# Kernel optimization log

Hardware: AMD Instinct MI355X
Metric: run time of the kernel (lower is better)

The kernel has to match this reference:

```python
import jax, jax.numpy as jnp
import numpy as np

NUM_HEADS = 16
HEAD_DIM = 64
EMBED_DIM = 1024
MASKED_BIAS = -10000.0


def setup_inputs() -> dict:
    key = jax.random.key(0)
    ks = jax.random.split(key, 4)
    B, S, D = 4, 1024, EMBED_DIM
    scale = 0.02
    return {
        "hidden_states": jax.random.normal(ks[0], (B, S, D), dtype=jnp.float32),
        "c_attn_w": jax.random.normal(ks[1], (D, 3 * D), dtype=jnp.float32) * scale,
        "c_attn_b": jnp.zeros((3 * D,), dtype=jnp.float32),
        "c_proj_w": jax.random.normal(ks[2], (D, D), dtype=jnp.float32) * scale,
        "c_proj_b": jnp.zeros((D,), dtype=jnp.float32),
        "affine_w": jnp.ones((D,), dtype=jnp.float32),
        "affine_b": jnp.zeros((D,), dtype=jnp.float32),
    }


def reference(hidden_states, c_attn_w, c_attn_b, c_proj_w, c_proj_b, affine_w, affine_b):
    B, S, D = hidden_states.shape
    H, Dh = NUM_HEADS, HEAD_DIM
    # c_attn (GPT2 Conv1D): x @ W + b -> [B,S,3D], split into q,k,v
    qkv = hidden_states @ c_attn_w + c_attn_b
    q, k, v = jnp.split(qkv, 3, axis=-1)
    # split heads -> [B,H,S,Dh]
    def split_heads(t):
        return t.reshape(B, S, H, Dh).transpose(0, 2, 1, 3)
    q, k, v = split_heads(q), split_heads(k), split_heads(v)
    # QK^T scaled by 1/sqrt(head_dim) (value.size(-1)**0.5)
    attn_weights = jnp.einsum("bhqd,bhkd->bhqk", q, k) / jnp.asarray(
        Dh, hidden_states.dtype) ** 0.5
    # causal mask via where with -10000 sentinel (eager GPT2 semantics)
    causal = jnp.tril(jnp.ones((S, S), dtype=bool))[None, None]
    attn_weights = jnp.where(causal, attn_weights,
                             jnp.asarray(MASKED_BIAS, attn_weights.dtype))
    attn_weights = jax.nn.softmax(attn_weights, axis=-1)
    # attn dropout = identity in eval
    attn_output = jnp.einsum("bhqk,bhkd->bhqd", attn_weights, v)
    # merge heads -> [B,S,D]
    attn_output = attn_output.transpose(0, 2, 1, 3).reshape(B, S, D)
    # c_proj (Conv1D), resid dropout identity, then affine
    attn_output = attn_output @ c_proj_w + c_proj_b
    attn_output = attn_output * affine_w + affine_b
    return attn_output
```

## Files before the change

kernel.cpp:

```cpp
#include <hip/hip_runtime.h>


typedef __attribute__((ext_vector_type(4))) float  fx4;
typedef __attribute__((ext_vector_type(4))) short  sx4;
typedef __attribute__((ext_vector_type(8))) short  sx8;
typedef __attribute__((ext_vector_type(4))) float  f32x4;
typedef __attribute__((ext_vector_type(8))) __bf16 bf16x8;

#define DEVI static __device__ __forceinline__
#define BARRIER asm volatile("s_barrier" ::: "memory")
#define VMCNT0  asm volatile("s_waitcnt vmcnt(0)" ::: "memory")

DEVI short f2bf(float f) {
  unsigned u = __builtin_bit_cast(unsigned, f);
  u = (u + 0x7FFFu + ((u >> 16) & 1u)) >> 16;
  return (short)u;
}

DEVI fx4 mfma16(sx8 a, sx8 b, fx4 c) {
  return __builtin_amdgcn_mfma_f32_16x16x32_bf16(
      __builtin_bit_cast(bf16x8, a), __builtin_bit_cast(bf16x8, b), c, 0, 0, 0);
}

DEVI void gl_lds16(const void* g, void* l) {
  __builtin_amdgcn_global_load_lds(
      (const __attribute__((address_space(1))) void*)g,
      (__attribute__((address_space(3))) void*)l, 16, 0, 0);
}

__global__ __launch_bounds__(256) void prologue(
    const float* __restrict__ hs, short* __restrict__ hsb,
    const float* __restrict__ caw, short* __restrict__ wqkvt,
    const float* __restrict__ cpw, short* __restrict__ wprojt) {
  __shared__ float tbuf[32][33];
  const int bid = blockIdx.x, tid = threadIdx.x;
  if (bid < 4096) {
    const float* in;
    short* out;
    int C, bx, by;
    if (bid < 3072) {
      in = caw; out = wqkvt; C = 3072; bx = bid % 96; by = bid / 96;
    } else {
      int t = bid - 3072;
      in = cpw; out = wprojt; C = 1024; bx = t & 31; by = t >> 5;
    }
    const int R = 1024;
    int tx = tid & 31, ty = tid >> 5;
    int r0 = by * 32, c0 = bx * 32;
#pragma unroll
    for (int i = 0; i < 4; ++i)
      tbuf[ty + i * 8][tx] = in[(size_t)(r0 + ty + i * 8) * C + c0 + tx];
    __syncthreads();
#pragma unroll
    for (int i = 0; i < 4; ++i)
      out[(size_t)(c0 + ty + i * 8) * R + r0 + tx] = f2bf(tbuf[tx][ty + i * 8]);
  } else {
    int i = (bid - 4096) * 256 + tid;
    f32x4 v = *(const f32x4*)&hs[(size_t)i * 4];
    sx4 o;
#pragma unroll
    for (int j = 0; j < 4; ++j) o[j] = f2bf(v[j]);
    *(sx4*)&hsb[(size_t)i * 4] = o;
  }
}

__global__ __launch_bounds__(512, 4) void gemm_qkv(
    const short* __restrict__ A, const short* __restrict__ Bt,
    const float* __restrict__ bias, short* __restrict__ Qg,
    short* __restrict__ Kg, short* __restrict__ Vtg) {
  __shared__ __align__(16) short As[2][64][64];
  __shared__ __align__(16) short Bs[2][128][64];
  const int tid = threadIdx.x, lane = tid & 63, w = tid >> 6;
  const int bid = blockIdx.x;
  const int x = bid & 7, loc = bid >> 3;
  const int bn = (x & 3) * 3 + loc % 3;
  const int bm = (x >> 2) * 16 + loc / 3;
  const int wm = w >> 2, wn = w & 3;
  const int c0 = lane & 15, g = lane >> 4;
  const int l3 = lane >> 3, l7 = lane & 7;
  const int slog = l7 ^ l3;
  const int par = slog >> 2, gg = slog & 3;
  const int K = 1024;
  fx4 acc[4][4] = {};

  auto STAGE = [&](int bf, int kt) {
    {
      int row = w * 16 + l3 * 2 + par;
      gl_lds16(&A[(size_t)(bm * 128 + row) * K + kt + gg * 8], &As[bf][w * 8][0]);
    }
#pragma unroll
    for (int i = 0; i < 2; ++i) {
      int ch = w * 2 + i;
      int row = ch * 16 + l3 * 2 + par;
      gl_lds16(&Bt[(size_t)(bn * 256 + row) * K + kt + gg * 8], &Bs[bf][ch * 8][0]);
    }
  };

  STAGE(0, 0);
  VMCNT0;
  BARRIER;
  for (int t = 0; t < 32; ++t) {
    const int bf = t & 1;
    if (t + 1 < 32) STAGE(bf ^ 1, (t + 1) * 32);

    sx8 af[4], bfr[4];
#pragma unroll
    for (int m = 0; m < 4; ++m) {
      int r = wm * 64 + m * 16 + c0, pr = r >> 1;
      int sl = (((r & 1) << 2) | g) ^ (pr & 7);
      af[m] = *(const sx8*)&As[bf][pr][sl * 8];
    }
#pragma unroll
    for (int n = 0; n < 4; ++n) {
      int r = wn * 64 + n * 16 + c0, pr = r >> 1;
      int sl = (((r & 1) << 2) | g) ^ (pr & 7);
      bfr[n] = *(const sx8*)&Bs[bf][pr][sl * 8];
    }
    __builtin_amdgcn_s_setprio(1);
#pragma unroll
    for (int m = 0; m < 4; ++m)
#pragma unroll
      for (int n = 0; n < 4; ++n) acc[m][n] = mfma16(af[m], bfr[n], acc[m][n]);
    __builtin_amdgcn_s_setprio(0);

    if (t + 1 < 32) {
      VMCNT0;
      BARRIER;
    }
  }

  const float SCALE_Q = 0.125f * 1.4426950408889634f;
#pragma unroll
  for (int m = 0; m < 4; ++m) {
#pragma unroll
    for (int n = 0; n < 4; ++n) {
      int col = bn * 256 + wn * 64 + n * 16 + c0;
      int row0 = bm * 128 + wm * 64 + m * 16 + g * 4;
      float bv = bias[col];
      int b = row0 >> 10, s0 = row0 & 1023;
      if (col < 1024) {
        int h = col >> 6, d = col & 63;
        size_t base = ((size_t)(b * 16 + h) * 1024) * 64 + d;
#pragma unroll
        for (int r = 0; r < 4; ++r)
          Qg[base + (size_t)(s0 + r) * 64] = f2bf((acc[m][n][r] + bv) * SCALE_Q);
      } else if (col < 2048) {
        int c = col - 1024, h = c >> 6, d = c & 63;
        size_t base = ((size_t)(b * 16 + h) * 1024) * 64 + d;
#pragma unroll
        for (int r = 0; r < 4; ++r)
          Kg[base + (size_t)(s0 + r) * 64] = f2bf(acc[m][n][r] + bv);
      } else {
        int c = col - 2048, h = c >> 6, d = c & 63;
        sx4 v;
#pragma unroll
        for (int r = 0; r < 4; ++r) v[r] = f2bf(acc[m][n][r] + bv);
        *(sx4*)&Vtg[((size_t)(b * 16 + h) * 64 + d) * 1024 + s0] = v;
      }
    }
  }
}

__global__ __launch_bounds__(512, 4) void gemm_proj(
    const short* __restrict__ A, const short* __restrict__ Bt,
    const float* __restrict__ bias, const float* __restrict__ aw,
    const float* __restrict__ ab, float* __restrict__ Out) {
  __shared__ __align__(16) short As[2][128][64];
  __shared__ __align__(16) short Bs[2][128][64];
  const int tid = threadIdx.x, lane = tid & 63, w = tid >> 6;
  const int bid = blockIdx.x;
  const int x = bid & 7, k = bid >> 3;
  const int bn = x, bm = k;
  const int wm = w >> 2, wn = w & 3;
  const int c0 = lane & 15, g = lane >> 4;
  const int lr8 = lane >> 3, ls8 = (lane & 7) ^ lr8;
  const int K = 1024, N = 1024;
  fx4 acc[4][2] = {};

  auto STAGE = [&](int bf, int kt) {
#pragma unroll
    for (int i = 0; i < 2; ++i) {
      int idx = w * 2 + i;
      gl_lds16(&A[(size_t)(bm * 128 + idx * 8 + lr8) * K + kt + ls8 * 8],
               &As[bf][idx * 8][0]);
      gl_lds16(&Bt[(size_t)(bn * 128 + idx * 8 + lr8) * K + kt + ls8 * 8],
               &Bs[bf][idx * 8][0]);
    }
  };

  STAGE(0, 0);
  VMCNT0;
  BARRIER;
  for (int t = 0; t < 16; ++t) {
    const int bf = t & 1;
    if (t + 1 < 16) STAGE(bf ^ 1, (t + 1) * 64);
#pragma unroll
    for (int kk = 0; kk < 2; ++kk) {
      sx8 af[4], bfr[2];
      int sb = kk * 4 + g;
#pragma unroll
      for (int m = 0; m < 4; ++m) {
        int row = wm * 64 + m * 16 + c0;
        af[m] = *(const sx8*)&As[bf][row][(sb ^ (row & 7)) * 8];
      }
#pragma unroll
      for (int n = 0; n < 2; ++n) {
        int row = wn * 32 + n * 16 + c0;
        bfr[n] = *(const sx8*)&Bs[bf][row][(sb ^ (row & 7)) * 8];
      }
#pragma unroll
      for (int m = 0; m < 4; ++m)
#pragma unroll
        for (int n = 0; n < 2; ++n) acc[m][n] = mfma16(af[m], bfr[n], acc[m][n]);
    }
    if (t + 1 < 16) {
      VMCNT0;
      BARRIER;
    }
  }

#pragma unroll
  for (int m = 0; m < 4; ++m) {
#pragma unroll
    for (int n = 0; n < 2; ++n) {
      int col = bn * 128 + wn * 32 + n * 16 + c0;
      int row0 = bm * 128 + wm * 64 + m * 16 + g * 4;
      float bv = bias[col], wv = aw[col], av = ab[col];
#pragma unroll
      for (int r = 0; r < 4; ++r)
        Out[(size_t)(row0 + r) * N + col] = (acc[m][n][r] + bv) * wv + av;
    }
  }
}

__global__ __launch_bounds__(256, 4) void attn_kernel(const short* __restrict__ Qg,
                                                      const short* __restrict__ Kg,
                                                      const short* __restrict__ Vtg,
                                                      short* __restrict__ AO) {
  __shared__ __align__(16) short Ks[2][64][64];
  __shared__ __align__(16) short Vts[2][64][64];
  __shared__ __align__(16) short Ps[4][16 * 64];
  const int tid = threadIdx.x, lane = tid & 63, w = tid >> 6;
  const int bid = blockIdx.x;
  const int u = bid >> 8, v = bid & 255, bh = v >> 2, jj = v & 3;
  const int qt = (u == 0) ? jj : (u == 1) ? 7 - jj : (u == 2) ? 8 + jj : 15 - jj;
  const int b = bh >> 4, h = bh & 15;
  const int c0 = lane & 15, g = lane >> 4;
  const int lr8 = lane >> 3, ls8 = (lane & 7) ^ lr8;
  const int q0 = qt * 64 + w * 16;
  const short* Qp = Qg + (size_t)bh * 65536;
  const short* Kp = Kg + (size_t)bh * 65536;
  const short* Vp = Vtg + (size_t)bh * 65536;
  short* pbase = &Ps[w][0];
  const int s8 = (c0 & 7) * 8;

  sx8 qf[2];
#pragma unroll
  for (int kk = 0; kk < 2; ++kk)
    qf[kk] = *(const sx8*)&Qp[(size_t)(q0 + c0) * 64 + kk * 32 + g * 8];

  fx4 o[4] = {};
  float mrun = -1e30f, lrun = 0.f;
  const int q_glob = q0 + c0;

  auto STAGE = [&](int bf, int kv0) {
#pragma unroll
    for (int i = 0; i < 2; ++i) {
      int idx = w * 2 + i;
      gl_lds16(&Kp[(size_t)(kv0 + idx * 8 + lr8) * 64 + ls8 * 8], &Ks[bf][idx * 8][0]);
    }
#pragma unroll
    for (int i = 0; i < 2; ++i) {
      int idx = w * 2 + i;
      gl_lds16(&Vp[(size_t)(idx * 8 + lr8) * 1024 + kv0 + ls8 * 8], &Vts[bf][idx * 8][0]);
    }
  };

  STAGE(0, 0);
  VMCNT0;
  BARRIER;
  for (int t = 0; t <= qt; ++t) {
    const int kv0 = t * 64;
    const int bf = t & 1;
    const bool more = t < qt;
    if (more) STAGE(bf ^ 1, kv0 + 64);

    fx4 st[4];
    __builtin_amdgcn_s_setprio(1);
#pragma unroll
    for (int mf = 0; mf < 4; ++mf) {
      int row = mf * 16 + c0;
      sx8 kf0 = *(const sx8*)&Ks[bf][row][(g ^ (row & 7)) * 8];
      sx8 kf1 = *(const sx8*)&Ks[bf][row][((4 + g) ^ (row & 7)) * 8];
      fx4 z = {0.f, 0.f, 0.f, 0.f};
      z = mfma16(kf0, qf[0], z);
      st[mf] = mfma16(kf1, qf[1], z);
    }
    __builtin_amdgcn_s_setprio(0);

    float pmax = -1e30f;
    if (t == qt) {
#pragma unroll
      for (int mf = 0; mf < 4; ++mf)
#pragma unroll
        for (int r = 0; r < 4; ++r) {
          int kv = kv0 + mf * 16 + g * 4 + r;
          float z = (kv > q_glob) ? -1e30f : st[mf][r];
          st[mf][r] = z;
          pmax = fmaxf(pmax, z);
        }
    } else {
#pragma unroll
      for (int mf = 0; mf < 4; ++mf)
#pragma unroll
        for (int r = 0; r < 4; ++r) pmax = fmaxf(pmax, st[mf][r]);
    }
    pmax = fmaxf(pmax, __shfl_xor(pmax, 16));
    pmax = fmaxf(pmax, __shfl_xor(pmax, 32));
    float mnew = fmaxf(mrun, pmax);
    float alpha = __builtin_amdgcn_exp2f(mrun - mnew);
    float psum = 0.f;
#pragma unroll
    for (int mf = 0; mf < 4; ++mf) {
      sx4 pv;
#pragma unroll
      for (int r = 0; r < 4; ++r) {
        float pp = __builtin_amdgcn_exp2f(st[mf][r] - mnew);
        psum += pp;
        pv[r] = f2bf(pp);
      }
      *(sx4*)&pbase[c0 * 64 + ((mf * 16 + g * 4) ^ s8)] = pv;
    }
    psum += __shfl_xor(psum, 16);
    psum += __shfl_xor(psum, 32);
    lrun = lrun * alpha + psum;
    mrun = mnew;
#pragma unroll
    for (int mf = 0; mf < 4; ++mf) o[mf] *= alpha;

    __builtin_amdgcn_s_setprio(1);
#pragma unroll
    for (int kk = 0; kk < 2; ++kk) {
      sx8 pbf = *(const sx8*)&pbase[c0 * 64 + ((kk * 32 + g * 8) ^ s8)];
#pragma unroll
      for (int mf = 0; mf < 4; ++mf) {
        int row = mf * 16 + c0;
        sx8 vaf = *(const sx8*)&Vts[bf][row][((kk * 4 + g) ^ (row & 7)) * 8];
        o[mf] = mfma16(vaf, pbf, o[mf]);
      }
    }
    __builtin_amdgcn_s_setprio(0);

    if (more) {
      VMCNT0;
      BARRIER;
    }
  }

  float inv = 1.0f / lrun;
  int q = q0 + c0;
#pragma unroll
  for (int mf = 0; mf < 4; ++mf) {
    sx4 v4;
#pragma unroll
    for (int r = 0; r < 4; ++r) v4[r] = f2bf(o[mf][r] * inv);
    int d0 = mf * 16 + g * 4;
    *(sx4*)&AO[((size_t)(b * 1024 + q)) * 1024 + h * 64 + d0] = v4;
  }
}

extern "C" void kernel_launch(void* const* d_in, const int* in_sizes, int n_in,
                              void* d_out, int out_size, void* d_ws, size_t ws_size,
                              hipStream_t stream) {
  const float* hs  = (const float*)d_in[0];
  const float* caw = (const float*)d_in[1];
  const float* cab = (const float*)d_in[2];
  const float* cpw = (const float*)d_in[3];
  const float* cpb = (const float*)d_in[4];
  const float* afw = (const float*)d_in[5];
  const float* afb = (const float*)d_in[6];
  float* out = (float*)d_out;
  char* ws = (char*)d_ws;

  short* hsb    = (short*)(ws);
  short* ao     = (short*)(ws);
  short* wqkvt  = (short*)(ws + ((size_t)8  << 20));
  short* wprojt = (short*)(ws + ((size_t)14 << 20));
  short* Qg     = (short*)(ws + ((size_t)16 << 20));
  short* Kg     = (short*)(ws + ((size_t)24 << 20));
  short* Vtg    = (short*)(ws + ((size_t)32 << 20));

  prologue<<<8192, 256, 0, stream>>>(hs, hsb, caw, wqkvt, cpw, wprojt);
  gemm_qkv<<<384, 512, 0, stream>>>(hsb, wqkvt, cab, Qg, Kg, Vtg);
  attn_kernel<<<1024, 256, 0, stream>>>(Qg, Kg, Vtg, ao);
  gemm_proj<<<256, 512, 0, stream>>>(ao, wprojt, cpb, afw, afb, out);
}
```

Before: 92.51 us.

## Restructure QKV GEMM to 128x128 single-buffered tiles with BK=64

Rewrites the QKV projection GEMM from a 512-thread, 128x256 block tile with double-buffered BK=32 LDS staging to a 256-thread, 128x128 tile with a single LDS buffer and BK=64. The grid doubles to 768 blocks, and the per-row XOR swizzle is simplified. The aim is higher occupancy and more blocks per CU, with half as many K iterations. In exchange it loses the load/compute overlap of double buffering and the s_setprio hints, and each block reuses less of the B tile.

```diff
diff --git a/kernel.cpp b/kernel.cpp
--- a/kernel.cpp
+++ b/kernel.cpp
@@ -64,77 +64,60 @@
   }
 }
 
-__global__ __launch_bounds__(512, 4) void gemm_qkv(
+__global__ __launch_bounds__(256, 8) void gemm_qkv(
     const short* __restrict__ A, const short* __restrict__ Bt,
     const float* __restrict__ bias, short* __restrict__ Qg,
     short* __restrict__ Kg, short* __restrict__ Vtg) {
-  __shared__ __align__(16) short As[2][64][64];
-  __shared__ __align__(16) short Bs[2][128][64];
+  __shared__ __align__(16) short As[128][64];
+  __shared__ __align__(16) short Bs[128][64];
   const int tid = threadIdx.x, lane = tid & 63, w = tid >> 6;
   const int bid = blockIdx.x;
   const int x = bid & 7, loc = bid >> 3;
-  const int bn = (x & 3) * 3 + loc % 3;
-  const int bm = (x >> 2) * 16 + loc / 3;
-  const int wm = w >> 2, wn = w & 3;
+  const int bn = x * 3 + loc % 3;
+  const int bm = loc / 3;
+  const int wm = w >> 1, wn = w & 1;
   const int c0 = lane & 15, g = lane >> 4;
-  const int l3 = lane >> 3, l7 = lane & 7;
-  const int slog = l7 ^ l3;
-  const int par = slog >> 2, gg = slog & 3;
+  const int lr8 = lane >> 3;
+  const int ls8 = (lane & 7) ^ lr8;
   const int K = 1024;
   fx4 acc[4][4] = {};
 
-  auto STAGE = [&](int bf, int kt) {
-    {
-      int row = w * 16 + l3 * 2 + par;
-      gl_lds16(&A[(size_t)(bm * 128 + row) * K + kt + gg * 8], &As[bf][w * 8][0]);
-    }
-#pragma unroll
-    for (int i = 0; i < 2; ++i) {
-      int ch = w * 2 + i;
-      int row = ch * 16 + l3 * 2 + par;
-      gl_lds16(&Bt[(size_t)(bn * 256 + row) * K + kt + gg * 8], &Bs[bf][ch * 8][0]);
-    }
-  };
-
-  STAGE(0, 0);
-  VMCNT0;
-  BARRIER;
-  for (int t = 0; t < 32; ++t) {
-    const int bf = t & 1;
-    if (t + 1 < 32) STAGE(bf ^ 1, (t + 1) * 32);
-
-    sx8 af[4], bfr[4];
-#pragma unroll
-    for (int m = 0; m < 4; ++m) {
-      int r = wm * 64 + m * 16 + c0, pr = r >> 1;
-      int sl = (((r & 1) << 2) | g) ^ (pr & 7);
-      af[m] = *(const sx8*)&As[bf][pr][sl * 8];
-    }
+  for (int kt = 0; kt < K; kt += 64) {
+#pragma unroll
+    for (int i = 0; i < 4; ++i) {
+      int r = w * 32 + i * 8;
+      gl_lds16(&A[(size_t)(bm * 128 + r + lr8) * K + kt + ls8 * 8], &As[r][0]);
+      gl_lds16(&Bt[(size_t)(bn * 128 + r + lr8) * K + kt + ls8 * 8], &Bs[r][0]);
+    }
+    __syncthreads();
+#pragma unroll
+    for (int kk = 0; kk < 2; ++kk) {
+      sx8 af[4], bfr[4];
+      int sb = kk * 4 + g;
+#pragma unroll
+      for (int m = 0; m < 4; ++m) {
+        int row = wm * 64 + m * 16 + c0;
+        af[m] = *(const sx8*)&As[row][(sb ^ (row & 7)) * 8];
+      }
+#pragma unroll
+      for (int n = 0; n < 4; ++n) {
+        int row = wn * 64 + n * 16 + c0;
+        bfr[n] = *(const sx8*)&Bs[row][(sb ^ (row & 7)) * 8];
+      }
+#pragma unroll
+      for (int m = 0; m < 4; ++m)
+#pragma unroll
+        for (int n = 0; n < 4; ++n) acc[m][n] = mfma16(af[m], bfr[n], acc[m][n]);
+    }
+    __syncthreads();
+  }
+
+  const float SCALE_Q = 0.125f * 1.4426950408889634f;
+#pragma unroll
+  for (int m = 0; m < 4; ++m) {
 #pragma unroll
     for (int n = 0; n < 4; ++n) {
-      int r = wn * 64 + n * 16 + c0, pr = r >> 1;
-      int sl = (((r & 1) << 2) | g) ^ (pr & 7);
-      bfr[n] = *(const sx8*)&Bs[bf][pr][sl * 8];
-    }
-    __builtin_amdgcn_s_setprio(1);
-#pragma unroll
-    for (int m = 0; m < 4; ++m)
-#pragma unroll
-      for (int n = 0; n < 4; ++n) acc[m][n] = mfma16(af[m], bfr[n], acc[m][n]);
-    __builtin_amdgcn_s_setprio(0);
-
-    if (t + 1 < 32) {
-      VMCNT0;
-      BARRIER;
-    }
-  }
-
-  const float SCALE_Q = 0.125f * 1.4426950408889634f;
-#pragma unroll
-  for (int m = 0; m < 4; ++m) {
-#pragma unroll
-    for (int n = 0; n < 4; ++n) {
-      int col = bn * 256 + wn * 64 + n * 16 + c0;
+      int col = bn * 128 + wn * 64 + n * 16 + c0;
       int row0 = bm * 128 + wm * 64 + m * 16 + g * 4;
       float bv = bias[col];
       int b = row0 >> 10, s0 = row0 & 1023;
@@ -391,7 +374,7 @@
   short* Vtg    = (short*)(ws + ((size_t)32 << 20));
 
   prologue<<<8192, 256, 0, stream>>>(hs, hsb, caw, wqkvt, cpw, wprojt);
-  gemm_qkv<<<384, 512, 0, stream>>>(hsb, wqkvt, cab, Qg, Kg, Vtg);
+  gemm_qkv<<<768, 256, 0, stream>>>(hsb, wqkvt, cab, Qg, Kg, Vtg);
   attn_kernel<<<1024, 256, 0, stream>>>(Qg, Kg, Vtg, ao);
   gemm_proj<<<256, 512, 0, stream>>>(ao, wprojt, cpb, afw, afb, out);
 }
```

New measurement: 100.4 us. 1.08x slower.
